# Kernel optimization log

Hardware: AMD Instinct MI355X
Metric: run time of the kernel (lower is better)

The kernel has to match this reference:

```python
import jax, jax.numpy as jnp
import numpy as np

HEADS = 16
EPS = 1e-5  # torch LayerNorm default


def _ln(x, s, b):
    m = jnp.mean(x, axis=-1, keepdims=True)
    v = jnp.mean((x - m) ** 2, axis=-1, keepdims=True)
    return (x - m) * jax.lax.rsqrt(v + EPS) * s + b


def setup_inputs() -> dict:
    key = jax.random.key(0)
    B, N, D, DEPTH, MLP = 2, 1024, 1024, 6, 4096
    ks = jax.random.split(key, 6)
    s = 0.02  # init scale so activations stay well-conditioned
    return {
        "x": jax.random.normal(ks[0], (B, N, D), dtype=jnp.float32),
        "ln1_s": jnp.ones((DEPTH, D), jnp.float32),
        "ln1_b": jnp.zeros((DEPTH, D), jnp.float32),
        "w_qkv": jax.random.normal(ks[1], (DEPTH, D, 3 * D), dtype=jnp.float32) * s,
        "w_out": jax.random.normal(ks[2], (DEPTH, D, D), dtype=jnp.float32) * s,
        "b_out": jnp.zeros((DEPTH, D), jnp.float32),
        "ln2_s": jnp.ones((DEPTH, D), jnp.float32),
        "ln2_b": jnp.zeros((DEPTH, D), jnp.float32),
        "w1": jax.random.normal(ks[3], (DEPTH, D, MLP), dtype=jnp.float32) * s,
        "b1": jnp.zeros((DEPTH, MLP), jnp.float32),
        "w2": jax.random.normal(ks[4], (DEPTH, MLP, D), dtype=jnp.float32) * s,
        "b2": jnp.zeros((DEPTH, D), jnp.float32),
    }


def reference(x, ln1_s, ln1_b, w_qkv, w_out, b_out, ln2_s, ln2_b, w1, b1, w2, b2):
    D = x.shape[-1]
    dh = D // HEADS
    scale = D ** -0.5  # NOTE: original scales by full dim**-0.5, not head_dim

    def layer(xc, p):
        l1s, l1b, wq, wo, bo, l2s, l2b, W1, B1, W2, B2 = p
        h = _ln(xc, l1s, l1b)
        b, n, _ = h.shape
        qkv = (h @ wq).reshape(b, n, 3, HEADS, dh)  # 'b n (qkv h d)' split order
        q = qkv[:, :, 0].transpose(0, 2, 1, 3)  # bhnd
        k = qkv[:, :, 1].transpose(0, 2, 1, 3)
        v = qkv[:, :, 2].transpose(0, 2, 1, 3)
        dots = jnp.einsum('bhid,bhjd->bhij', q, k) * scale
        attn = jax.nn.softmax(dots, axis=-1)
        o = jnp.einsum('bhij,bhjd->bhid', attn, v)
        o = o.transpose(0, 2, 1, 3).reshape(b, n, D)
        xc = xc + (o @ wo + bo)  # Residual(PreNorm(Attention))
        h2 = _ln(xc, l2s, l2b)
        xc = xc + (jax.nn.gelu(h2 @ W1 + B1, approximate=False) @ W2 + B2)
        return xc, None

    x, _ = jax.lax.scan(layer, x, (ln1_s, ln1_b, w_qkv, w_out, b_out,
                                   ln2_s, ln2_b, w1, b1, w2, b2))
    return x
```

## Files before the change

kernel.cpp:

```cpp
#include <hip/hip_runtime.h>
#include <math.h>

typedef unsigned short ushort_t;
typedef __bf16 bf16x8 __attribute__((ext_vector_type(8)));
typedef float f32x4 __attribute__((ext_vector_type(4)));

#define HEADS 16

__device__ __forceinline__ ushort_t f2b(float f) {
    unsigned int u = __float_as_uint(f);
    unsigned int r = (u + 0x7FFFu + ((u >> 16) & 1u)) >> 16;
    return (ushort_t)r;
}

__device__ __forceinline__ void g2lds(const void* g, void* l) {
    __builtin_amdgcn_global_load_lds(
        (const __attribute__((address_space(1))) unsigned int*)g,
        (__attribute__((address_space(3))) unsigned int*)l, 16, 0, 0);
}

__global__ __launch_bounds__(256) void copy_kernel(const float* __restrict__ x,
                                                   float* __restrict__ y) {
    int i = blockIdx.x * 256 + threadIdx.x;
    ((float4*)y)[i] = ((const float4*)x)[i];
}

__global__ __launch_bounds__(256) void transpose_kernel(const float* __restrict__ W,
                                                        ushort_t* __restrict__ Wt,
                                                        int K, int N) {
    __shared__ ushort_t sT[64 * 72];
    const int t = threadIdx.x;
    const int k0 = blockIdx.y * 64;
    const int n0 = blockIdx.x * 64;
    const int kk = t >> 4;
    const int nc = (t & 15) * 4;
#pragma unroll
    for (int i = 0; i < 4; i++) {
        int k = kk + i * 16;
        float4 v = *(const float4*)(W + (size_t)(k0 + k) * N + n0 + nc);
        const float* vf = (const float*)&v;
#pragma unroll
        for (int j = 0; j < 4; j++) sT[(nc + j) * 72 + k] = f2b(vf[j]);
    }
    __syncthreads();
#pragma unroll
    for (int p = 0; p < 2; p++) {
        int u = t + p * 256;
        int n = u >> 3;
        int kc = (u & 7) * 8;
        *(uint4*)(Wt + (size_t)(n0 + n) * K + k0 + kc) = *(const uint4*)(sT + n * 72 + kc);
    }
}

__global__ __launch_bounds__(256) void ln_kernel(const float* __restrict__ x,
                                                 const float* __restrict__ s,
                                                 const float* __restrict__ b,
                                                 ushort_t* __restrict__ out) {
    int row = blockIdx.x;
    int t = threadIdx.x;
    const float* xr = x + (size_t)row * 1024;
    float4 xv = *(const float4*)(xr + t * 4);
    float sum = xv.x + xv.y + xv.z + xv.w;
    float sq = xv.x * xv.x + xv.y * xv.y + xv.z * xv.z + xv.w * xv.w;
#pragma unroll
    for (int m = 1; m < 64; m <<= 1) {
        sum += __shfl_xor(sum, m);
        sq += __shfl_xor(sq, m);
    }
    __shared__ float red[8];
    int wave = t >> 6, lane = t & 63;
    if (lane == 0) { red[wave] = sum; red[4 + wave] = sq; }
    __syncthreads();
    sum = red[0] + red[1] + red[2] + red[3];
    sq = red[4] + red[5] + red[6] + red[7];
    float mean = sum * (1.0f / 1024.0f);
    float var = sq * (1.0f / 1024.0f) - mean * mean;
    float inv = rsqrtf(var + 1e-5f);
    float4 sv = *(const float4*)(s + t * 4);
    float4 bv = *(const float4*)(b + t * 4);
    unsigned int lo = (unsigned int)f2b((xv.x - mean) * inv * sv.x + bv.x) |
                      ((unsigned int)f2b((xv.y - mean) * inv * sv.y + bv.y) << 16);
    unsigned int hi = (unsigned int)f2b((xv.z - mean) * inv * sv.z + bv.z) |
                      ((unsigned int)f2b((xv.w - mean) * inv * sv.w + bv.w) << 16);
    uint2 o;
    o.x = lo; o.y = hi;
    *(uint2*)(out + (size_t)row * 1024 + t * 4) = o;
}

template <int MODE, int BN>
__global__ __launch_bounds__(256) void gemm_bt_kernel(
    const ushort_t* __restrict__ A, const ushort_t* __restrict__ Bt,
    const float* __restrict__ bias, float* __restrict__ res,
    ushort_t* __restrict__ outb, ushort_t* __restrict__ qo,
    ushort_t* __restrict__ ko, ushort_t* __restrict__ vto, int K, int N) {
    constexpr int NF = BN / 32;
    constexpr int PB = BN / 32;
    __shared__ __align__(16) ushort_t sA[2][128 * 64];
    __shared__ __align__(16) ushort_t sB[2][BN * 64];
    const int t = threadIdx.x;
    const int lane = t & 63;
    const int wave = t >> 6;
    const int l15 = lane & 15;
    const int quad = lane >> 4;
    const int wm = wave >> 1, wn = wave & 1;
    const int m0 = blockIdx.y * 128;
    const int n0 = blockIdx.x * BN;

    f32x4 acc[4][NF];
#pragma unroll
    for (int i = 0; i < 4; i++)
#pragma unroll
        for (int j = 0; j < NF; j++) acc[i][j] = (f32x4){0.f, 0.f, 0.f, 0.f};

    const int rlow = lane >> 3;
    const int chunk = (lane & 7) ^ rlow;
    const int rowS = wave * 8 + rlow;
    const ushort_t* gA = A + (size_t)(m0 + rowS) * K + chunk * 8;
    const ushort_t* gB = Bt + (size_t)(n0 + rowS) * K + chunk * 8;
    const int lslot = wave * 512;
    const int xorv = l15 & 7;

    const int nkt = K >> 6;
#pragma unroll
    for (int p = 0; p < 4; p++) g2lds(gA + (size_t)p * 32 * K, &sA[0][0] + lslot + p * 2048);
#pragma unroll
    for (int p = 0; p < PB; p++) g2lds(gB + (size_t)p * 32 * K, &sB[0][0] + lslot + p * 2048);

    int cur = 0;
    for (int kt = 0; kt < nkt; kt++) {
        __syncthreads();
        if (kt + 1 < nkt) {
            const size_t koff = (size_t)(kt + 1) * 64;
            const int nxt = cur ^ 1;
#pragma unroll
            for (int p = 0; p < 4; p++)
                g2lds(gA + (size_t)p * 32 * K + koff, &sA[nxt][0] + lslot + p * 2048);
#pragma unroll
            for (int p = 0; p < PB; p++)
                g2lds(gB + (size_t)p * 32 * K + koff, &sB[nxt][0] + lslot + p * 2048);
        }
#pragma unroll
        for (int ks = 0; ks < 2; ks++) {
            const int co = ((ks * 4 + quad) ^ xorv) * 8;
            bf16x8 af[4], bf[NF];
#pragma unroll
            for (int i = 0; i < 4; i++)
                af[i] = *(const bf16x8*)(&sA[cur][0] + (wm * 64 + i * 16 + l15) * 64 + co);
#pragma unroll
            for (int i = 0; i < NF; i++)
                bf[i] = *(const bf16x8*)(&sB[cur][0] + (wn * (BN / 2) + i * 16 + l15) * 64 + co);
#pragma unroll
            for (int mi = 0; mi < 4; mi++)
#pragma unroll
                for (int ni = 0; ni < NF; ni++)
                    acc[mi][ni] = __builtin_amdgcn_mfma_f32_16x16x32_bf16(
                        af[mi], bf[ni], acc[mi][ni], 0, 0, 0);
        }
        cur ^= 1;
    }
#pragma unroll
    for (int mi = 0; mi < 4; mi++) {
#pragma unroll
        for (int ni = 0; ni < NF; ni++) {
#pragma unroll
            for (int r = 0; r < 4; r++) {
                int mg = m0 + wm * 64 + mi * 16 + quad * 4 + r;
                int ng = n0 + wn * (BN / 2) + ni * 16 + l15;
                float c = acc[mi][ni][r];
                if (MODE == 1) {
                    size_t idx = (size_t)mg * N + ng;
                    res[idx] = res[idx] + c + bias[ng];
                } else if (MODE == 2) {
                    float vv = c + bias[ng];
                    float g = 0.5f * vv * (1.0f + erff(vv * 0.70710678118654752f));
                    outb[(size_t)mg * N + ng] = f2b(g);
                } else {
                    int qkv = ng >> 10;
                    int rem = ng & 1023;
                    int hh = rem >> 6;
                    int dd = rem & 63;
                    int bb = mg >> 10;
                    int seq = mg & 1023;
                    ushort_t val = f2b(c);
                    if (qkv == 0)
                        qo[((size_t)(bb * HEADS + hh) * 1024 + seq) * 64 + dd] = val;
                    else if (qkv == 1)
                        ko[((size_t)(bb * HEADS + hh) * 1024 + seq) * 64 + dd] = val;
                    else
                        vto[((size_t)(bb * HEADS + hh) * 64 + dd) * 1024 + seq] = val;
                }
            }
        }
    }
}

__global__ __launch_bounds__(256) void attn_kernel(const ushort_t* __restrict__ q,
                                                   const ushort_t* __restrict__ k,
                                                   const ushort_t* __restrict__ vt,
                                                   ushort_t* __restrict__ o) {
    __shared__ __align__(16) ushort_t sK[64 * 72];
    __shared__ __align__(16) ushort_t sV[64 * 72];
    __shared__ __align__(16) ushort_t sP[4 * 16 * 72];
    const int t = threadIdx.x;
    const int lane = t & 63;
    const int w = t >> 6;
    const int l15 = lane & 15;
    const int quad = lane >> 4;
    const int qt = blockIdx.x;
    const int bh = blockIdx.y;

    bf16x8 aq[2];
    const ushort_t* qbase = q + ((size_t)bh * 1024 + qt * 64 + w * 16 + l15) * 64;
    aq[0] = *(const bf16x8*)(qbase + quad * 8);
    aq[1] = *(const bf16x8*)(qbase + 32 + quad * 8);

    float m_old[4], l_sum[4];
    f32x4 oacc[4];
#pragma unroll
    for (int r = 0; r < 4; r++) { m_old[r] = -1e30f; l_sum[r] = 0.f; }
#pragma unroll
    for (int i = 0; i < 4; i++) oacc[i] = (f32x4){0.f, 0.f, 0.f, 0.f};

    const float scale = 0.03125f;

    for (int kt = 0; kt < 16; kt++) {
        __syncthreads();
#pragma unroll
        for (int p = 0; p < 2; p++) {
            int u = t + p * 256;
            int row = u >> 3, ch = u & 7;
            uint4 v = *(const uint4*)(k + ((size_t)bh * 1024 + kt * 64 + row) * 64 + ch * 8);
            *(uint4*)(sK + row * 72 + ch * 8) = v;
            uint4 v2 = *(const uint4*)(vt + ((size_t)bh * 64 + row) * 1024 + kt * 64 + ch * 8);
            *(uint4*)(sV + row * 72 + ch * 8) = v2;
        }
        __syncthreads();
        f32x4 s[4];
#pragma unroll
        for (int nt = 0; nt < 4; nt++) {
            f32x4 a = (f32x4){0.f, 0.f, 0.f, 0.f};
#pragma unroll
            for (int ks = 0; ks < 2; ks++) {
                bf16x8 bk = *(const bf16x8*)(sK + (nt * 16 + l15) * 72 + ks * 32 + quad * 8);
                a = __builtin_amdgcn_mfma_f32_16x16x32_bf16(aq[ks], bk, a, 0, 0, 0);
            }
            s[nt] = a * scale;
        }
        float alpha[4];
#pragma unroll
        for (int r = 0; r < 4; r++) {
            float mx = fmaxf(fmaxf(s[0][r], s[1][r]), fmaxf(s[2][r], s[3][r]));
#pragma unroll
            for (int msk = 1; msk < 16; msk <<= 1) mx = fmaxf(mx, __shfl_xor(mx, msk));
            float mnew = fmaxf(m_old[r], mx);
            alpha[r] = __expf(m_old[r] - mnew);
            float psum = 0.f;
#pragma unroll
            for (int nt = 0; nt < 4; nt++) {
                float p = __expf(s[nt][r] - mnew);
                s[nt][r] = p;
                psum += p;
            }
#pragma unroll
            for (int msk = 1; msk < 16; msk <<= 1) psum += __shfl_xor(psum, msk);
            l_sum[r] = l_sum[r] * alpha[r] + psum;
            m_old[r] = mnew;
        }
#pragma unroll
        for (int i = 0; i < 4; i++)
#pragma unroll
            for (int r = 0; r < 4; r++) oacc[i][r] *= alpha[r];
#pragma unroll
        for (int nt = 0; nt < 4; nt++)
#pragma unroll
            for (int r = 0; r < 4; r++)
                sP[w * 1152 + (quad * 4 + r) * 72 + nt * 16 + l15] = f2b(s[nt][r]);
        __syncthreads();
#pragma unroll
        for (int nt = 0; nt < 4; nt++) {
#pragma unroll
            for (int ks = 0; ks < 2; ks++) {
                bf16x8 ap = *(const bf16x8*)(sP + w * 1152 + l15 * 72 + ks * 32 + quad * 8);
                bf16x8 bv = *(const bf16x8*)(sV + (nt * 16 + l15) * 72 + ks * 32 + quad * 8);
                oacc[nt] = __builtin_amdgcn_mfma_f32_16x16x32_bf16(ap, bv, oacc[nt], 0, 0, 0);
            }
        }
    }
    int b = bh >> 4, hh = bh & 15;
#pragma unroll
    for (int nt = 0; nt < 4; nt++)
#pragma unroll
        for (int r = 0; r < 4; r++) {
            int row = qt * 64 + w * 16 + quad * 4 + r;
            float val = oacc[nt][r] / l_sum[r];
            o[((size_t)b * 1024 + row) * 1024 + hh * 64 + nt * 16 + l15] = f2b(val);
        }
}

extern "C" void kernel_launch(void* const* d_in, const int* in_sizes, int n_in,
                              void* d_out, int out_size, void* d_ws, size_t ws_size,
                              hipStream_t stream) {
    const float* x = (const float*)d_in[0];
    const float* ln1_s = (const float*)d_in[1];
    const float* ln1_b = (const float*)d_in[2];
    const float* w_qkv = (const float*)d_in[3];
    const float* w_out = (const float*)d_in[4];
    const float* b_out = (const float*)d_in[5];
    const float* ln2_s = (const float*)d_in[6];
    const float* ln2_b = (const float*)d_in[7];
    const float* w1 = (const float*)d_in[8];
    const float* b1 = (const float*)d_in[9];
    const float* w2 = (const float*)d_in[10];
    const float* b2 = (const float*)d_in[11];

    float* res = (float*)d_out;
    char* wsb = (char*)d_ws;
    const size_t MB = 1024 * 1024;
    ushort_t* h = (ushort_t*)(wsb + 0 * MB);
    ushort_t* qb = (ushort_t*)(wsb + 4 * MB);
    ushort_t* kb = (ushort_t*)(wsb + 8 * MB);
    ushort_t* vtb = (ushort_t*)(wsb + 12 * MB);
    ushort_t* ob = (ushort_t*)(wsb + 16 * MB);
    ushort_t* ub = (ushort_t*)(wsb + 4 * MB);
    ushort_t* wqkv_t = (ushort_t*)(wsb + 20 * MB);
    ushort_t* wo_t = (ushort_t*)(wsb + 26 * MB);
    ushort_t* w12_t = (ushort_t*)(wsb + 20 * MB);

    copy_kernel<<<2048, 256, 0, stream>>>(x, res);
    for (int l = 0; l < 6; l++) {
        transpose_kernel<<<dim3(48, 16), 256, 0, stream>>>(
            w_qkv + (size_t)l * 1024 * 3072, wqkv_t, 1024, 3072);
        transpose_kernel<<<dim3(16, 16), 256, 0, stream>>>(
            w_out + (size_t)l * 1024 * 1024, wo_t, 1024, 1024);
        ln_kernel<<<2048, 256, 0, stream>>>(res, ln1_s + l * 1024, ln1_b + l * 1024, h);
        gemm_bt_kernel<0, 128><<<dim3(24, 16, 1), 256, 0, stream>>>(
            h, wqkv_t, nullptr, nullptr, nullptr, qb, kb, vtb, 1024, 3072);
        attn_kernel<<<dim3(16, 32), 256, 0, stream>>>(qb, kb, vtb, ob);
        gemm_bt_kernel<1, 64><<<dim3(16, 16, 1), 256, 0, stream>>>(
            ob, wo_t, b_out + l * 1024, res, nullptr, nullptr, nullptr, nullptr,
            1024, 1024);
        transpose_kernel<<<dim3(64, 16), 256, 0, stream>>>(
            w1 + (size_t)l * 1024 * 4096, w12_t, 1024, 4096);
        ln_kernel<<<2048, 256, 0, stream>>>(res, ln2_s + l * 1024, ln2_b + l * 1024, h);
        gemm_bt_kernel<2, 128><<<dim3(32, 16, 1), 256, 0, stream>>>(
            h, w12_t, b1 + l * 4096, nullptr, ub, nullptr, nullptr, nullptr,
            1024, 4096);
        transpose_kernel<<<dim3(16, 64), 256, 0, stream>>>(
            w2 + (size_t)l * 4096 * 1024, w12_t, 4096, 1024);
        gemm_bt_kernel<1, 64><<<dim3(16, 16, 1), 256, 0, stream>>>(
            ub, w12_t, b2 + l * 1024, res, nullptr, nullptr, nullptr, nullptr,
            4096, 1024);
    }
}
```

Measured before the change: 1.487 ms.

## Split-K the residual GEMMs and remap workgroups across XCDs

The out-projection and MLP-down GEMMs, which launch only 256 workgroups, gain a grid z dimension that splits K. Slice 0 adds its result into the residual while the other slices write fp32 partials to workspace. The partials are summed inside the next LayerNorm kernel, with a final reduce kernel after the last layer. All GEMM and attention workgroups also get a blockIdx remap that spreads consecutive tiles across the 8 XCDs for better L2 locality. The cost is extra partial-sum traffic and a dependence on workspace size to pick the split factor.

```diff
diff --git a/kernel.cpp b/kernel.cpp
--- a/kernel.cpp
+++ b/kernel.cpp
@@ -6,6 +6,7 @@
 typedef float f32x4 __attribute__((ext_vector_type(4)));
 
 #define HEADS 16
+#define RES_ELEMS ((size_t)2048 * 1024)
 
 __device__ __forceinline__ ushort_t f2b(float f) {
     unsigned int u = __float_as_uint(f);
@@ -52,14 +53,20 @@
     }
 }
 
-__global__ __launch_bounds__(256) void ln_kernel(const float* __restrict__ x,
+__global__ __launch_bounds__(256) void ln_kernel(float* __restrict__ x,
+                                                 const float* __restrict__ part, int np,
                                                  const float* __restrict__ s,
                                                  const float* __restrict__ b,
                                                  ushort_t* __restrict__ out) {
     int row = blockIdx.x;
     int t = threadIdx.x;
-    const float* xr = x + (size_t)row * 1024;
-    float4 xv = *(const float4*)(xr + t * 4);
+    size_t off = (size_t)row * 1024 + t * 4;
+    float4 xv = *(const float4*)(x + off);
+    for (int p = 0; p < np; p++) {
+        float4 pv = *(const float4*)(part + (size_t)p * RES_ELEMS + off);
+        xv.x += pv.x; xv.y += pv.y; xv.z += pv.z; xv.w += pv.w;
+    }
+    if (np > 0) *(float4*)(x + off) = xv;
     float sum = xv.x + xv.y + xv.z + xv.w;
     float sq = xv.x * xv.x + xv.y * xv.y + xv.z * xv.z + xv.w * xv.w;
 #pragma unroll
@@ -87,10 +94,22 @@
     *(uint2*)(out + (size_t)row * 1024 + t * 4) = o;
 }
 
+__global__ __launch_bounds__(256) void reduce_kernel(float* __restrict__ res,
+                                                     const float* __restrict__ part, int np) {
+    size_t i = ((size_t)blockIdx.x * 256 + threadIdx.x) * 4;
+    float4 a = *(const float4*)(res + i);
+    for (int p = 0; p < np; p++) {
+        float4 pv = *(const float4*)(part + (size_t)p * RES_ELEMS + i);
+        a.x += pv.x; a.y += pv.y; a.z += pv.z; a.w += pv.w;
+    }
+    *(float4*)(res + i) = a;
+}
+
 template <int MODE, int BN>
 __global__ __launch_bounds__(256) void gemm_bt_kernel(
     const ushort_t* __restrict__ A, const ushort_t* __restrict__ Bt,
     const float* __restrict__ bias, float* __restrict__ res,
+    float* __restrict__ part,
     ushort_t* __restrict__ outb, ushort_t* __restrict__ qo,
     ushort_t* __restrict__ ko, ushort_t* __restrict__ vto, int K, int N) {
     constexpr int NF = BN / 32;
@@ -103,8 +122,20 @@
     const int l15 = lane & 15;
     const int quad = lane >> 4;
     const int wm = wave >> 1, wn = wave & 1;
-    const int m0 = blockIdx.y * 128;
-    const int n0 = blockIdx.x * BN;
+
+    const int gx = gridDim.x, gy = gridDim.y, gz = gridDim.z;
+    const int nwg = gx * gy * gz;
+    const int L = blockIdx.x + gx * (blockIdx.y + gy * blockIdx.z);
+    const int f = (L & 7) * (nwg >> 3) + (L >> 3);
+    const int bx = f % gx;
+    const int fq = f / gx;
+    const int by = fq % gy;
+    const int bz = fq / gy;
+
+    const int m0 = by * 128;
+    const int n0 = bx * BN;
+    const int Ks = K / gz;
+    const int kbeg = bz * Ks;
 
     f32x4 acc[4][NF];
 #pragma unroll
@@ -115,12 +146,12 @@
     const int rlow = lane >> 3;
     const int chunk = (lane & 7) ^ rlow;
     const int rowS = wave * 8 + rlow;
-    const ushort_t* gA = A + (size_t)(m0 + rowS) * K + chunk * 8;
-    const ushort_t* gB = Bt + (size_t)(n0 + rowS) * K + chunk * 8;
+    const ushort_t* gA = A + (size_t)(m0 + rowS) * K + kbeg + chunk * 8;
+    const ushort_t* gB = Bt + (size_t)(n0 + rowS) * K + kbeg + chunk * 8;
     const int lslot = wave * 512;
     const int xorv = l15 & 7;
 
-    const int nkt = K >> 6;
+    const int nkt = Ks >> 6;
 #pragma unroll
     for (int p = 0; p < 4; p++) g2lds(gA + (size_t)p * 32 * K, &sA[0][0] + lslot + p * 2048);
 #pragma unroll
@@ -169,7 +200,10 @@
                 float c = acc[mi][ni][r];
                 if (MODE == 1) {
                     size_t idx = (size_t)mg * N + ng;
-                    res[idx] = res[idx] + c + bias[ng];
+                    if (bz == 0)
+                        res[idx] = res[idx] + c + bias[ng];
+                    else
+                        part[(size_t)(bz - 1) * RES_ELEMS + idx] = c;
                 } else if (MODE == 2) {
                     float vv = c + bias[ng];
                     float g = 0.5f * vv * (1.0f + erff(vv * 0.70710678118654752f));
@@ -206,8 +240,10 @@
     const int w = t >> 6;
     const int l15 = lane & 15;
     const int quad = lane >> 4;
-    const int qt = blockIdx.x;
-    const int bh = blockIdx.y;
+    const int L = blockIdx.x + 16 * blockIdx.y;
+    const int f = (L & 7) * 64 + (L >> 3);
+    const int qt = f & 15;
+    const int bh = f >> 4;
 
     bf16x8 aq[2];
     const ushort_t* qbase = q + ((size_t)bh * 1024 + qt * 64 + w * 16 + l15) * 64;
@@ -326,29 +362,49 @@
     ushort_t* wo_t = (ushort_t*)(wsb + 26 * MB);
     ushort_t* w12_t = (ushort_t*)(wsb + 20 * MB);
 
+    int zwo, zml;
+    float* part_wo;
+    float* part_ml;
+    if (ws_size >= 52 * MB) {
+        zwo = 4; zml = 4;
+        part_wo = (float*)(wsb + 28 * MB);
+        part_ml = (float*)(wsb + 28 * MB);
+    } else if (ws_size >= 36 * MB) {
+        zwo = 2; zml = 2;
+        part_wo = (float*)(wsb + 4 * MB);
+        part_ml = (float*)(wsb + 28 * MB);
+    } else {
+        zwo = 2; zml = 1;
+        part_wo = (float*)(wsb + 4 * MB);
+        part_ml = nullptr;
+    }
+
     copy_kernel<<<2048, 256, 0, stream>>>(x, res);
     for (int l = 0; l < 6; l++) {
         transpose_kernel<<<dim3(48, 16), 256, 0, stream>>>(
             w_qkv + (size_t)l * 1024 * 3072, wqkv_t, 1024, 3072);
         transpose_kernel<<<dim3(16, 16), 256, 0, stream>>>(
             w_out + (size_t)l * 1024 * 1024, wo_t, 1024, 1024);
-        ln_kernel<<<2048, 256, 0, stream>>>(res, ln1_s + l * 1024, ln1_b + l * 1024, h);
+        ln_kernel<<<2048, 256, 0, stream>>>(res, part_ml, l == 0 ? 0 : zml - 1,
+                                            ln1_s + l * 1024, ln1_b + l * 1024, h);
         gemm_bt_kernel<0, 128><<<dim3(24, 16, 1), 256, 0, stream>>>(
-            h, wqkv_t, nullptr, nullptr, nullptr, qb, kb, vtb, 1024, 3072);
+            h, wqkv_t, nullptr, nullptr, nullptr, nullptr, qb, kb, vtb, 1024, 3072);
         attn_kernel<<<dim3(16, 32), 256, 0, stream>>>(qb, kb, vtb, ob);
-        gemm_bt_kernel<1, 64><<<dim3(16, 16, 1), 256, 0, stream>>>(
-            ob, wo_t, b_out + l * 1024, res, nullptr, nullptr, nullptr, nullptr,
+        gemm_bt_kernel<1, 64><<<dim3(16, 16, zwo), 256, 0, stream>>>(
+            ob, wo_t, b_out + l * 1024, res, part_wo, nullptr, nullptr, nullptr, nullptr,
             1024, 1024);
         transpose_kernel<<<dim3(64, 16), 256, 0, stream>>>(
             w1 + (size_t)l * 1024 * 4096, w12_t, 1024, 4096);
-        ln_kernel<<<2048, 256, 0, stream>>>(res, ln2_s + l * 1024, ln2_b + l * 1024, h);
+        ln_kernel<<<2048, 256, 0, stream>>>(res, part_wo, zwo - 1,
+                                            ln2_s + l * 1024, ln2_b + l * 1024, h);
         gemm_bt_kernel<2, 128><<<dim3(32, 16, 1), 256, 0, stream>>>(
-            h, w12_t, b1 + l * 4096, nullptr, ub, nullptr, nullptr, nullptr,
+            h, w12_t, b1 + l * 4096, nullptr, nullptr, ub, nullptr, nullptr, nullptr,
             1024, 4096);
         transpose_kernel<<<dim3(16, 64), 256, 0, stream>>>(
             w2 + (size_t)l * 4096 * 1024, w12_t, 4096, 1024);
-        gemm_bt_kernel<1, 64><<<dim3(16, 16, 1), 256, 0, stream>>>(
-            ub, w12_t, b2 + l * 1024, res, nullptr, nullptr, nullptr, nullptr,
+        gemm_bt_kernel<1, 64><<<dim3(16, 16, zml), 256, 0, stream>>>(
+            ub, w12_t, b2 + l * 1024, res, part_ml, nullptr, nullptr, nullptr, nullptr,
             4096, 1024);
     }
-}
+    if (zml > 1) reduce_kernel<<<2048, 256, 0, stream>>>(res, part_ml, zml - 1);
+}
```

After: 1.521 ms. 2.3% more time.

## Triple-buffer GEMM LDS pipeline and remap workgroups across XCDs

Applied to the files above, without the earlier changes.

Moves the GEMM kernel from double to triple buffering in LDS. Loads are now prefetched two k-tiles ahead, with an explicit vmcnt wait and a raw s_barrier in place of __syncthreads. Both the GEMM and attention kernels also remap workgroup IDs so that neighbouring tiles land on the same XCD, which should improve L2 reuse. The costs are higher LDS use, which may lower occupancy, and a remap that assumes the workgroup count is divisible by 8.

```diff
diff --git a/kernel.cpp b/kernel.cpp
--- a/kernel.cpp
+++ b/kernel.cpp
@@ -95,16 +95,24 @@
     ushort_t* __restrict__ ko, ushort_t* __restrict__ vto, int K, int N) {
     constexpr int NF = BN / 32;
     constexpr int PB = BN / 32;
-    __shared__ __align__(16) ushort_t sA[2][128 * 64];
-    __shared__ __align__(16) ushort_t sB[2][BN * 64];
+    __shared__ __align__(16) ushort_t sA[3][128 * 64];
+    __shared__ __align__(16) ushort_t sB[3][BN * 64];
     const int t = threadIdx.x;
     const int lane = t & 63;
     const int wave = t >> 6;
     const int l15 = lane & 15;
     const int quad = lane >> 4;
     const int wm = wave >> 1, wn = wave & 1;
-    const int m0 = blockIdx.y * 128;
-    const int n0 = blockIdx.x * BN;
+
+    const int gx = gridDim.x, gy = gridDim.y;
+    const int nwg = gx * gy;
+    const int L = blockIdx.x + gx * blockIdx.y;
+    const int f = (L & 7) * (nwg >> 3) + (L >> 3);
+    const int bx = f % gx;
+    const int by = f / gx;
+
+    const int m0 = by * 128;
+    const int n0 = bx * BN;
 
     f32x4 acc[4][NF];
 #pragma unroll
@@ -122,33 +130,49 @@
 
     const int nkt = K >> 6;
 #pragma unroll
-    for (int p = 0; p < 4; p++) g2lds(gA + (size_t)p * 32 * K, &sA[0][0] + lslot + p * 2048);
-#pragma unroll
-    for (int p = 0; p < PB; p++) g2lds(gB + (size_t)p * 32 * K, &sB[0][0] + lslot + p * 2048);
-
-    int cur = 0;
+    for (int b2 = 0; b2 < 2; b2++) {
+#pragma unroll
+        for (int p = 0; p < 4; p++)
+            g2lds(gA + (size_t)p * 32 * K + b2 * 64, &sA[b2][0] + lslot + p * 2048);
+#pragma unroll
+        for (int p = 0; p < PB; p++)
+            g2lds(gB + (size_t)p * 32 * K + b2 * 64, &sB[b2][0] + lslot + p * 2048);
+    }
+
     for (int kt = 0; kt < nkt; kt++) {
-        __syncthreads();
         if (kt + 1 < nkt) {
-            const size_t koff = (size_t)(kt + 1) * 64;
-            const int nxt = cur ^ 1;
-#pragma unroll
-            for (int p = 0; p < 4; p++)
-                g2lds(gA + (size_t)p * 32 * K + koff, &sA[nxt][0] + lslot + p * 2048);
-#pragma unroll
-            for (int p = 0; p < PB; p++)
-                g2lds(gB + (size_t)p * 32 * K + koff, &sB[nxt][0] + lslot + p * 2048);
-        }
+            if constexpr (BN == 128)
+                asm volatile("s_waitcnt vmcnt(8)" ::: "memory");
+            else
+                asm volatile("s_waitcnt vmcnt(6)" ::: "memory");
+        } else {
+            asm volatile("s_waitcnt vmcnt(0)" ::: "memory");
+        }
+        __builtin_amdgcn_sched_barrier(0);
+        __builtin_amdgcn_s_barrier();
+        __builtin_amdgcn_sched_barrier(0);
+        if (kt + 2 < nkt) {
+            const size_t koff = (size_t)(kt + 2) * 64;
+            const int nb = (kt + 2) % 3;
+            ushort_t* dA = &sA[nb][0] + lslot;
+            ushort_t* dB = &sB[nb][0] + lslot;
+#pragma unroll
+            for (int p = 0; p < 4; p++) g2lds(gA + (size_t)p * 32 * K + koff, dA + p * 2048);
+#pragma unroll
+            for (int p = 0; p < PB; p++) g2lds(gB + (size_t)p * 32 * K + koff, dB + p * 2048);
+        }
+        const ushort_t* cA = &sA[kt % 3][0];
+        const ushort_t* cB = &sB[kt % 3][0];
 #pragma unroll
         for (int ks = 0; ks < 2; ks++) {
             const int co = ((ks * 4 + quad) ^ xorv) * 8;
             bf16x8 af[4], bf[NF];
 #pragma unroll
             for (int i = 0; i < 4; i++)
-                af[i] = *(const bf16x8*)(&sA[cur][0] + (wm * 64 + i * 16 + l15) * 64 + co);
+                af[i] = *(const bf16x8*)(cA + (wm * 64 + i * 16 + l15) * 64 + co);
 #pragma unroll
             for (int i = 0; i < NF; i++)
-                bf[i] = *(const bf16x8*)(&sB[cur][0] + (wn * (BN / 2) + i * 16 + l15) * 64 + co);
+                bf[i] = *(const bf16x8*)(cB + (wn * (BN / 2) + i * 16 + l15) * 64 + co);
 #pragma unroll
             for (int mi = 0; mi < 4; mi++)
 #pragma unroll
@@ -156,7 +180,7 @@
                     acc[mi][ni] = __builtin_amdgcn_mfma_f32_16x16x32_bf16(
                         af[mi], bf[ni], acc[mi][ni], 0, 0, 0);
         }
-        cur ^= 1;
+        __builtin_amdgcn_sched_barrier(0);
     }
 #pragma unroll
     for (int mi = 0; mi < 4; mi++) {
@@ -206,8 +230,10 @@
     const int w = t >> 6;
     const int l15 = lane & 15;
     const int quad = lane >> 4;
-    const int qt = blockIdx.x;
-    const int bh = blockIdx.y;
+    const int L = blockIdx.x + 16 * blockIdx.y;
+    const int f = (L & 7) * 64 + (L >> 3);
+    const int qt = f & 15;
+    const int bh = f >> 4;
 
     bf16x8 aq[2];
     const ushort_t* qbase = q + ((size_t)bh * 1024 + qt * 64 + w * 16 + l15) * 64;
```

New measurement: 1.711 ms. +15.0%, slower.
